# Performance work log

Hardware: AMD Instinct MI355X
Metric: run time of the kernel (lower is better)

Reference implementation:

```python
import jax, jax.numpy as jnp
import numpy as np

B, S, E, H, F = 8, 1024, 1024, 16, 4096
D = E // H  # head_dim = 64
EPS = 1e-5


def setup_inputs() -> dict:
    key = jax.random.key(0)
    ks = jax.random.split(key, 12)
    s = 0.02
    return {
        "x": jax.random.normal(ks[0], (B, S, E), dtype=jnp.float32),
        # per-head projections (shared across heads), torch stores [out,in]; we use [in,out]
        "Wq": jax.random.normal(ks[1], (D, D), dtype=jnp.float32) * s,
        "Wk": jax.random.normal(ks[2], (D, D), dtype=jnp.float32) * s,
        "Wv": jax.random.normal(ks[3], (D, D), dtype=jnp.float32) * s,
        "Wo": jax.random.normal(ks[4], (E, E), dtype=jnp.float32) * s,
        "bo": jnp.zeros((E,), dtype=jnp.float32),
        "W1": jax.random.normal(ks[5], (E, F), dtype=jnp.float32) * s,
        "b1": jnp.zeros((F,), dtype=jnp.float32),
        "W2": jax.random.normal(ks[6], (F, E), dtype=jnp.float32) * s,
        "b2": jnp.zeros((E,), dtype=jnp.float32),
        "g1": jnp.ones((E,), dtype=jnp.float32),
        "beta1": jnp.zeros((E,), dtype=jnp.float32),
        "g2": jnp.ones((E,), dtype=jnp.float32),
        "beta2": jnp.zeros((E,), dtype=jnp.float32),
    }


def _layer_norm(x, g, b):
    m = jnp.mean(x, axis=-1, keepdims=True)
    v = jnp.mean(jnp.square(x - m), axis=-1, keepdims=True)
    return (x - m) * jax.lax.rsqrt(v + EPS) * g + b


def reference(x, Wq, Wk, Wv, Wo, bo, W1, b1, W2, b2, g1, beta1, g2, beta2):
    b, s, e = x.shape
    # --- attention sublayer (pre-norm) ---
    nx = _layer_norm(x, g1, beta1)
    h = nx.reshape(b, s, H, D)              # [B,S,H,D]
    q = h @ Wq                               # per-head linear, weight shared over heads
    k = h @ Wk
    v = h @ Wv
    energy = jnp.einsum('bqhd,bkhd->bhqk', q, k)  # full [B,H,S,S] scores
    mask = jnp.tril(jnp.ones((s, s), dtype=bool))
    energy = jnp.where(mask, energy, -jnp.inf)
    att = jax.nn.softmax(energy / jnp.sqrt(jnp.float32(e)), axis=-1)  # NOTE: scale by sqrt(embed_dim)
    o = jnp.einsum('bhqk,bkhd->bqhd', att, v).reshape(b, s, e)
    x = x + (o @ Wo + bo)
    # --- MLP sublayer (pre-norm); dropout is identity in eval ---
    nx = _layer_norm(x, g2, beta2)
    x = x + (jax.nn.relu(nx @ W1 + b1) @ W2 + b2)
    return x
```

## Files before the change

kernel.cpp:

```cpp
#include <hip/hip_runtime.h>

typedef unsigned short u16;
typedef __attribute__((ext_vector_type(4))) float f4;
typedef __attribute__((ext_vector_type(8))) short s8v;
typedef __attribute__((ext_vector_type(4))) unsigned short u16x4;

#define DEVINL __device__ __forceinline__

DEVINL float b2f(u16 u) { union { unsigned i; float f; } x; x.i = ((unsigned)u) << 16; return x.f; }
DEVINL u16 f2b(float f) {
  union { float f; unsigned i; } x; x.f = f;
  unsigned r = 0x7FFFu + ((x.i >> 16) & 1u);
  return (u16)((x.i + r) >> 16);
}

#define GLD_LDS16(g, l)                                                        \
  __builtin_amdgcn_global_load_lds((__attribute__((address_space(1))) void*)(g), \
                                   (__attribute__((address_space(3))) void*)(l), 16, 0, 0)

__global__ __launch_bounds__(256) void k_transpose_all(
    const float* __restrict__ Wo, const float* __restrict__ W1,
    const float* __restrict__ W2, const float* __restrict__ Wq,
    const float* __restrict__ Wk, const float* __restrict__ Wv,
    u16* __restrict__ WoT, u16* __restrict__ W1T, u16* __restrict__ W2T,
    u16* __restrict__ WqT, u16* __restrict__ WkT, u16* __restrict__ WvT) {
  int id = blockIdx.x;
  const float* in;
  u16* out;
  int R, C, bx, by;
  if (id < 1024) {
    in = Wo; out = WoT; R = 1024; C = 1024; bx = id & 31; by = id >> 5;
  } else if (id < 5120) {
    int t = id - 1024;
    in = W1; out = W1T; R = 1024; C = 4096; bx = t & 127; by = t >> 7;
  } else if (id < 9216) {
    int t = id - 5120;
    in = W2; out = W2T; R = 4096; C = 1024; bx = t & 31; by = t >> 5;
  } else {
    int t = id - 9216;
    int z = t >> 2;
    in = z == 0 ? Wq : (z == 1 ? Wk : Wv);
    out = z == 0 ? WqT : (z == 1 ? WkT : WvT);
    R = 64; C = 64; bx = t & 1; by = (t >> 1) & 1;
  }
  __shared__ float tt[32][33];
  int tx = threadIdx.x & 31, ty = threadIdx.x >> 5;
  int c0 = bx * 32, r0 = by * 32;
#pragma unroll
  for (int i = 0; i < 32; i += 8)
    tt[ty + i][tx] = in[(long)(r0 + ty + i) * C + (c0 + tx)];
  __syncthreads();
#pragma unroll
  for (int i = 0; i < 32; i += 8)
    out[(long)(c0 + ty + i) * R + (r0 + tx)] = f2b(tt[tx][ty + i]);
}

__global__ __launch_bounds__(256) void k_vtrans(const u16* __restrict__ v, u16* __restrict__ vt) {
  __shared__ u16 t[64][72];
  int bh = blockIdx.x, b = bh >> 4, h = bh & 15;
  int s0 = blockIdx.y * 64;
  int tid = threadIdx.x;
#pragma unroll
  for (int p = 0; p < 2; ++p) {
    int idx = p * 256 + tid;
    int sl = idx >> 3, c8 = (idx & 7) * 8;
    *(s8v*)(&t[sl][c8]) = *(const s8v*)(v + (((long)(b * 1024 + s0 + sl) * 16 + h) * 64) + c8);
  }
  __syncthreads();
#pragma unroll
  for (int p = 0; p < 2; ++p) {
    int idx = p * 256 + tid;
    int d = idx >> 3, c8 = (idx & 7) * 8;
    s8v o;
#pragma unroll
    for (int e = 0; e < 8; ++e) o[e] = (short)t[c8 + e][d];
    *(s8v*)(vt + ((long)bh * 64 + d) * 1024 + s0 + c8) = o;
  }
}

__global__ __launch_bounds__(256) void k_layernorm(const float* __restrict__ x,
                                                   const float* __restrict__ g,
                                                   const float* __restrict__ be,
                                                   u16* __restrict__ out) {
  long row = blockIdx.x;
  int tid = threadIdx.x;
  f4 v = ((const f4*)(x + row * 1024))[tid];
  float s = v[0] + v[1] + v[2] + v[3];
  float s2 = v[0] * v[0] + v[1] * v[1] + v[2] * v[2] + v[3] * v[3];
#pragma unroll
  for (int off = 32; off > 0; off >>= 1) {
    s += __shfl_down(s, off, 64);
    s2 += __shfl_down(s2, off, 64);
  }
  __shared__ float red[8];
  int wv = tid >> 6, ln = tid & 63;
  if (ln == 0) { red[wv] = s; red[4 + wv] = s2; }
  __syncthreads();
  s = red[0] + red[1] + red[2] + red[3];
  s2 = red[4] + red[5] + red[6] + red[7];
  float mean = s * (1.0f / 1024.0f);
  float var = s2 * (1.0f / 1024.0f) - mean * mean;
  float rs = rsqrtf(var + 1e-5f);
  f4 gg = ((const f4*)g)[tid];
  f4 bb = ((const f4*)be)[tid];
  u16x4 o;
#pragma unroll
  for (int i = 0; i < 4; ++i) o[i] = f2b((v[i] - mean) * rs * gg[i] + bb[i]);
  ((u16x4*)(out + row * 1024))[tid] = o;
}

__global__ __launch_bounds__(256) void k_qkv(const u16* __restrict__ nx, const u16* __restrict__ WqT,
                                             const u16* __restrict__ WkT, const u16* __restrict__ WvT,
                                             u16* __restrict__ q, u16* __restrict__ k,
                                             u16* __restrict__ v) {
  int tid = threadIdx.x, lane = tid & 63, wave = tid >> 6;
  int quad = lane >> 4, l16 = lane & 15;
  long rbase = (long)blockIdx.x * 64 + wave * 16;
  s8v a0 = *(const s8v*)(nx + (rbase + l16) * 64 + quad * 8);
  s8v a1 = *(const s8v*)(nx + (rbase + l16) * 64 + 32 + quad * 8);
  const u16* Ws[3] = {WqT, WkT, WvT};
  u16* Os[3] = {q, k, v};
#pragma unroll
  for (int t = 0; t < 3; ++t) {
#pragma unroll
    for (int j = 0; j < 4; ++j) {
      s8v b0 = *(const s8v*)(Ws[t] + (j * 16 + l16) * 64 + quad * 8);
      s8v b1 = *(const s8v*)(Ws[t] + (j * 16 + l16) * 64 + 32 + quad * 8);
      f4 acc = {0.f, 0.f, 0.f, 0.f};
      acc = __builtin_amdgcn_mfma_f32_16x16x32_bf16(a0, b0, acc, 0, 0, 0);
      acc = __builtin_amdgcn_mfma_f32_16x16x32_bf16(a1, b1, acc, 0, 0, 0);
#pragma unroll
      for (int r = 0; r < 4; ++r)
        Os[t][(rbase + quad * 4 + r) * 64 + j * 16 + l16] = f2b(acc[r]);
    }
  }
}

__global__ __launch_bounds__(256) void k_attn_mfma(const u16* __restrict__ q,
                                                   const u16* __restrict__ kk,
                                                   const u16* __restrict__ vt,
                                                   u16* __restrict__ o) {
  constexpr int LDK = 72;
  __shared__ u16 Ks[64 * LDK];
  __shared__ u16 Vt[64 * LDK];
  __shared__ u16 Ps[4][16 * LDK];
  int tid = threadIdx.x, lane = tid & 63, wave = tid >> 6;
  int quad = lane >> 4, l16 = lane & 15;
  int b = blockIdx.x >> 4, h = blockIdx.x & 15;
  int qi = (int)gridDim.y - 1 - (int)blockIdx.y;
  int q0 = qi * 64 + wave * 16;

  const u16* qp = q + (((long)(b * 1024 + q0 + l16)) * 16 + h) * 64;
  s8v aq0 = *(const s8v*)(qp + quad * 8);
  s8v aq1 = *(const s8v*)(qp + 32 + quad * 8);

  f4 O[4];
  float m_[4], l_[4];
#pragma unroll
  for (int jd = 0; jd < 4; ++jd) O[jd] = f4{0.f, 0.f, 0.f, 0.f};
#pragma unroll
  for (int r = 0; r < 4; ++r) { m_[r] = -__builtin_inff(); l_[r] = 0.f; }

  for (int kt = 0; kt <= qi; ++kt) {
    __syncthreads();
#pragma unroll
    for (int p = 0; p < 2; ++p) {
      int idx = p * 256 + tid;
      int row = idx >> 3, c8 = (idx & 7) * 8;
      *(s8v*)(Ks + row * LDK + c8) =
          *(const s8v*)(kk + (((long)(b * 1024 + kt * 64 + row)) * 16 + h) * 64 + c8);
      *(s8v*)(Vt + row * LDK + c8) =
          *(const s8v*)(vt + ((long)blockIdx.x * 64 + row) * 1024 + kt * 64 + c8);
    }
    __syncthreads();

    f4 sf[4];
    __builtin_amdgcn_s_setprio(1);
#pragma unroll
    for (int jn = 0; jn < 4; ++jn) {
      s8v b0 = *(const s8v*)(Ks + (jn * 16 + l16) * LDK + quad * 8);
      s8v b1 = *(const s8v*)(Ks + (jn * 16 + l16) * LDK + 32 + quad * 8);
      f4 acc = f4{0.f, 0.f, 0.f, 0.f};
      acc = __builtin_amdgcn_mfma_f32_16x16x32_bf16(aq0, b0, acc, 0, 0, 0);
      acc = __builtin_amdgcn_mfma_f32_16x16x32_bf16(aq1, b1, acc, 0, 0, 0);
      sf[jn] = acc;
    }
    __builtin_amdgcn_s_setprio(0);
    bool diag = (kt == qi);
    float rm[4];
#pragma unroll
    for (int r = 0; r < 4; ++r) rm[r] = -__builtin_inff();
#pragma unroll
    for (int jn = 0; jn < 4; ++jn)
#pragma unroll
      for (int r = 0; r < 4; ++r) {
        float v = sf[jn][r] * 0.03125f;
        if (diag && (jn * 16 + l16 > wave * 16 + quad * 4 + r)) v = -__builtin_inff();
        sf[jn][r] = v;
        rm[r] = fmaxf(rm[r], v);
      }
#pragma unroll
    for (int off = 1; off < 16; off <<= 1)
#pragma unroll
      for (int r = 0; r < 4; ++r) rm[r] = fmaxf(rm[r], __shfl_xor(rm[r], off, 64));
    float alpha[4], rs[4];
#pragma unroll
    for (int r = 0; r < 4; ++r) {
      float mn = fmaxf(m_[r], rm[r]);
      alpha[r] = __expf(m_[r] - mn);
      m_[r] = mn;
      rs[r] = 0.f;
    }
#pragma unroll
    for (int jn = 0; jn < 4; ++jn)
#pragma unroll
      for (int r = 0; r < 4; ++r) {
        float p = __expf(sf[jn][r] - m_[r]);
        rs[r] += p;
        Ps[wave][(quad * 4 + r) * LDK + jn * 16 + l16] = f2b(p);
      }
#pragma unroll
    for (int off = 1; off < 16; off <<= 1)
#pragma unroll
      for (int r = 0; r < 4; ++r) rs[r] += __shfl_xor(rs[r], off, 64);
#pragma unroll
    for (int r = 0; r < 4; ++r) l_[r] = l_[r] * alpha[r] + rs[r];
#pragma unroll
    for (int jd = 0; jd < 4; ++jd)
#pragma unroll
      for (int r = 0; r < 4; ++r) O[jd][r] *= alpha[r];
    asm volatile("s_waitcnt lgkmcnt(0)" ::: "memory");
    s8v p0 = *(const s8v*)(&Ps[wave][l16 * LDK + quad * 8]);
    s8v p1 = *(const s8v*)(&Ps[wave][l16 * LDK + 32 + quad * 8]);
    __builtin_amdgcn_s_setprio(1);
#pragma unroll
    for (int jd = 0; jd < 4; ++jd) {
      s8v b0 = *(const s8v*)(Vt + (jd * 16 + l16) * LDK + quad * 8);
      s8v b1 = *(const s8v*)(Vt + (jd * 16 + l16) * LDK + 32 + quad * 8);
      O[jd] = __builtin_amdgcn_mfma_f32_16x16x32_bf16(p0, b0, O[jd], 0, 0, 0);
      O[jd] = __builtin_amdgcn_mfma_f32_16x16x32_bf16(p1, b1, O[jd], 0, 0, 0);
    }
    __builtin_amdgcn_s_setprio(0);
  }
#pragma unroll
  for (int r = 0; r < 4; ++r) {
    float inv = 1.0f / l_[r];
    u16* op = o + (((long)(b * 1024 + q0 + quad * 4 + r)) * 16 + h) * 64;
#pragma unroll
    for (int jd = 0; jd < 4; ++jd) op[jd * 16 + l16] = f2b(O[jd][r] * inv);
  }
}

template <int EPI>
__global__ __launch_bounds__(512) void k_gemm256(const u16* __restrict__ A,
                                                 const u16* __restrict__ BT,
                                                 const float* __restrict__ bias,
                                                 const float* __restrict__ resid,
                                                 void* __restrict__ outp, int M, int N, int K,
                                                 int lda) {
  __shared__ __align__(16) u16 S[65536];
  int tid = threadIdx.x, lane = tid & 63, wave = tid >> 6;
  int l16 = lane & 15, quad = lane >> 4;
  int wm = wave >> 2, wn = wave & 3;
  long bm = blockIdx.x, bn = blockIdx.y;
  int z = blockIdx.z;

  int rl = l16 & 7;
  int c0 = 8 * (quad ^ rl);
  int c1 = 8 * ((quad ^ 4) ^ rl);
  int rowA = (wm * 64 + l16) * 64;
  int rowB = (wn * 32 + l16) * 64;

  int Lb = tid * 16;
  int Ls = Lb ^ (((Lb >> 7) & 7) << 4);
  int r_ = Ls >> 7, kin = (Ls & 127) >> 1;
  const u16* pA = A + (bm * 256 + r_) * (long)lda + kin + (long)z * K;
  const u16* pB = BT + (bn * 256 + r_) * (long)lda + kin + (long)z * K;

  f4 acc[4][4][2];
#pragma unroll
  for (int q = 0; q < 4; ++q)
#pragma unroll
    for (int mi = 0; mi < 4; ++mi)
#pragma unroll
      for (int nj = 0; nj < 2; ++nj) acc[q][mi][nj] = f4{0.f, 0.f, 0.f, 0.f};
  s8v aF[4][2], bF[2][2][2];

#define BAR asm volatile("s_barrier" ::: "memory")
#define LGK0 asm volatile("s_waitcnt lgkmcnt(0)" ::: "memory")
#define WVM4 asm volatile("s_waitcnt vmcnt(4)" ::: "memory")
#define WVM0 asm volatile("s_waitcnt vmcnt(0)" ::: "memory")

#define STAGE(mat, half, t, buf)                                               \
  do {                                                                         \
    const u16* g_ = ((mat) ? pB : pA) + (long)(half) * 128 * lda + (t) * 64;   \
    char* l_ = ((char*)S) + ((buf) * 32768 + (mat) * 16384 + (half) * 8192) * 2 + wave * 1024; \
    GLD_LDS16(g_, l_);                                                         \
    GLD_LDS16(g_ + 64 * (long)lda, l_ + 8192);                                 \
  } while (0)

#define LDA(buf, mh)                                                           \
  do {                                                                         \
    const u16* p_ = S + (buf) * 32768 + (mh) * 8192 + rowA;                    \
    _Pragma("unroll") for (int mi = 0; mi < 4; ++mi) {                         \
      aF[mi][0] = *(const s8v*)(p_ + mi * 1024 + c0);                          \
      aF[mi][1] = *(const s8v*)(p_ + mi * 1024 + c1);                          \
    }                                                                          \
  } while (0)

#define LDB(buf, nh, set)                                                      \
  do {                                                                         \
    const u16* p_ = S + (buf) * 32768 + 16384 + (nh) * 8192 + rowB;            \
    _Pragma("unroll") for (int nj = 0; nj < 2; ++nj) {                         \
      bF[set][nj][0] = *(const s8v*)(p_ + nj * 1024 + c0);                     \
      bF[set][nj][1] = *(const s8v*)(p_ + nj * 1024 + c1);                     \
    }                                                                          \
  } while (0)

#define MM(q)                                                                  \
  do {                                                                         \
    _Pragma("unroll") for (int mi = 0; mi < 4; ++mi)                           \
        _Pragma("unroll") for (int nj = 0; nj < 2; ++nj) {                     \
      acc[q][mi][nj] = __builtin_amdgcn_mfma_f32_16x16x32_bf16(                \
          aF[mi][0], bF[(q) & 1][nj][0], acc[q][mi][nj], 0, 0, 0);             \
      acc[q][mi][nj] = __builtin_amdgcn_mfma_f32_16x16x32_bf16(                \
          aF[mi][1], bF[(q) & 1][nj][1], acc[q][mi][nj], 0, 0, 0);             \
    }                                                                          \
  } while (0)

#define PHASES(t, LAST)                                                        \
  LDA(0, 0); LDB(0, 0, 0); STAGE(0, 1, (t) + 1, 1);                            \
  BAR; LGK0; __builtin_amdgcn_s_setprio(1); MM(0); __builtin_amdgcn_s_setprio(0); BAR; \
  LDB(0, 1, 1); STAGE(1, 1, (t) + 1, 1);                                       \
  BAR; LGK0; __builtin_amdgcn_s_setprio(1); MM(1); __builtin_amdgcn_s_setprio(0); BAR; \
  LDA(0, 1); if (!(LAST)) STAGE(0, 0, (t) + 2, 0);                             \
  BAR; LGK0; __builtin_amdgcn_s_setprio(1); MM(2); __builtin_amdgcn_s_setprio(0); BAR; \
  if (!(LAST)) STAGE(1, 0, (t) + 2, 0);                                        \
  __builtin_amdgcn_s_setprio(1); MM(3); __builtin_amdgcn_s_setprio(0);         \
  if (LAST) { WVM0; } else { WVM4; }                                           \
  BAR;                                                                         \
  LDA(1, 0); LDB(1, 0, 0); if (!(LAST)) STAGE(0, 1, (t) + 2, 0);               \
  BAR; LGK0; __builtin_amdgcn_s_setprio(1); MM(0); __builtin_amdgcn_s_setprio(0); BAR; \
  LDB(1, 1, 1); if (!(LAST)) STAGE(1, 1, (t) + 2, 0);                          \
  BAR; LGK0; __builtin_amdgcn_s_setprio(1); MM(1); __builtin_amdgcn_s_setprio(0); BAR; \
  LDA(1, 1); if (!(LAST)) STAGE(0, 0, (t) + 3, 1);                             \
  BAR; LGK0; __builtin_amdgcn_s_setprio(1); MM(2); __builtin_amdgcn_s_setprio(0); BAR; \
  if (!(LAST)) STAGE(1, 0, (t) + 3, 1);                                        \
  __builtin_amdgcn_s_setprio(1); MM(3); __builtin_amdgcn_s_setprio(0);         \
  if (!(LAST)) { WVM4; BAR; }

  STAGE(0, 0, 0, 0);
  STAGE(1, 0, 0, 0);
  STAGE(0, 1, 0, 0);
  STAGE(1, 1, 0, 0);
  STAGE(0, 0, 1, 1);
  STAGE(1, 0, 1, 1);
  WVM4; BAR;

  int NI = K >> 7;
  for (int i = 0; i < NI - 1; ++i) {
    int t = 2 * i;
    PHASES(t, 0);
  }
  {
    int t = 2 * (NI - 1);
    PHASES(t, 1);
  }

#undef PHASES
#undef MM
#undef LDB
#undef LDA
#undef STAGE
#undef WVM0
#undef WVM4
#undef LGK0
#undef BAR

  float* P0 = (EPI == 0) ? ((float*)outp + (long)z * M * N) : nullptr;
#pragma unroll
  for (int q = 0; q < 4; ++q) {
    int mh = q >> 1, nh = q & 1;
#pragma unroll
    for (int mi = 0; mi < 4; ++mi) {
#pragma unroll
      for (int nj = 0; nj < 2; ++nj) {
        long row = bm * 256 + mh * 128 + wm * 64 + mi * 16 + quad * 4;
        int col = (int)bn * 256 + nh * 128 + wn * 32 + nj * 16 + l16;
        float bcol = 0.f;
        if (EPI != 0) bcol = bias[col];
#pragma unroll
        for (int rr = 0; rr < 4; ++rr) {
          float val = acc[q][mi][nj][rr] + bcol;
          if (EPI == 0) {
            P0[(row + rr) * (long)N + col] = val;
          } else if (EPI == 1) {
            ((u16*)outp)[(row + rr) * (long)N + col] = f2b(val > 0.f ? val : 0.f);
          } else {
            ((float*)outp)[(row + rr) * (long)N + col] =
                resid[(row + rr) * (long)N + col] + val;
          }
        }
      }
    }
  }
}

__global__ __launch_bounds__(512) void k_gemm256n128(const u16* __restrict__ A,
                                                     const u16* __restrict__ BT,
                                                     const float* __restrict__ bias,
                                                     const float* __restrict__ resid,
                                                     float* __restrict__ outp,
                                                     int M, int N, int K, int lda) {
  __shared__ __align__(16) u16 S[49152];
  int tid = threadIdx.x, lane = tid & 63, wave = tid >> 6;
  int l16 = lane & 15, quad = lane >> 4;
  int wm = wave >> 1, wn = wave & 1;
  long bm = blockIdx.x, bn = blockIdx.y;

  int rl = l16 & 7;
  int c0 = 8 * (quad ^ rl);
  int c1 = 8 * ((quad ^ 4) ^ rl);
  int rowA = (wm >> 1) * 8192 + ((wm & 1) * 64 + l16) * 64;
  int rowB = 16384 + (wn * 64 + l16) * 64;

  int Lb = tid * 16;
  int Ls = Lb ^ (((Lb >> 7) & 7) << 4);
  int r_ = Ls >> 7, kin = (Ls & 127) >> 1;
  const u16* pA = A + (bm * 256 + r_) * (long)lda + kin;
  const u16* pB = BT + (bn * 128 + r_) * (long)lda + kin;

  f4 acc[4][4];
#pragma unroll
  for (int mi = 0; mi < 4; ++mi)
#pragma unroll
    for (int nj = 0; nj < 4; ++nj) acc[mi][nj] = f4{0.f, 0.f, 0.f, 0.f};
  s8v aF[4][2], bF[2][2];

#define BAR asm volatile("s_barrier" ::: "memory")
#define LGK0 asm volatile("s_waitcnt lgkmcnt(0)" ::: "memory")
#define WVM4 asm volatile("s_waitcnt vmcnt(4)" ::: "memory")
#define WVM0 asm volatile("s_waitcnt vmcnt(0)" ::: "memory")

#define STAGEA(t, buf)                                                         \
  do {                                                                         \
    const u16* g_ = pA + (t) * 64;                                             \
    char* l_ = ((char*)S) + (buf) * 49152 + wave * 1024;                       \
    GLD_LDS16(g_, l_);                                                         \
    GLD_LDS16(g_ + 64 * (long)lda, l_ + 8192);                                 \
    GLD_LDS16(g_ + 128 * (long)lda, l_ + 16384);                               \
    GLD_LDS16(g_ + 192 * (long)lda, l_ + 24576);                               \
  } while (0)

#define STAGEB(t, buf)                                                         \
  do {                                                                         \
    const u16* g_ = pB + (t) * 64;                                             \
    char* l_ = ((char*)S) + (buf) * 49152 + 32768 + wave * 1024;               \
    GLD_LDS16(g_, l_);                                                         \
    GLD_LDS16(g_ + 64 * (long)lda, l_ + 8192);                                 \
  } while (0)

#define LDAn(buf)                                                              \
  do {                                                                         \
    const u16* p_ = S + (buf) * 24576 + rowA;                                  \
    _Pragma("unroll") for (int mi = 0; mi < 4; ++mi) {                         \
      aF[mi][0] = *(const s8v*)(p_ + mi * 1024 + c0);                          \
      aF[mi][1] = *(const s8v*)(p_ + mi * 1024 + c1);                          \
    }                                                                          \
  } while (0)

#define LDBn(buf, nh)                                                          \
  do {                                                                         \
    const u16* p_ = S + (buf) * 24576 + rowB + (nh) * 2048;                    \
    _Pragma("unroll") for (int nj2 = 0; nj2 < 2; ++nj2) {                      \
      bF[nj2][0] = *(const s8v*)(p_ + nj2 * 1024 + c0);                        \
      bF[nj2][1] = *(const s8v*)(p_ + nj2 * 1024 + c1);                        \
    }                                                                          \
  } while (0)

#define MMn(nh)                                                                \
  do {                                                                         \
    _Pragma("unroll") for (int mi = 0; mi < 4; ++mi)                           \
        _Pragma("unroll") for (int nj2 = 0; nj2 < 2; ++nj2) {                  \
      acc[mi][(nh) * 2 + nj2] = __builtin_amdgcn_mfma_f32_16x16x32_bf16(       \
          aF[mi][0], bF[nj2][0], acc[mi][(nh) * 2 + nj2], 0, 0, 0);            \
      acc[mi][(nh) * 2 + nj2] = __builtin_amdgcn_mfma_f32_16x16x32_bf16(       \
          aF[mi][1], bF[nj2][1], acc[mi][(nh) * 2 + nj2], 0, 0, 0);            \
    }                                                                          \
  } while (0)

#define PHASES(t, LAST)                                                        \
  LDAn(0); LDBn(0, 0); STAGEB((t) + 1, 1);                                     \
  BAR; LGK0; __builtin_amdgcn_s_setprio(1); MMn(0); __builtin_amdgcn_s_setprio(0); BAR; \
  LDBn(0, 1); if (!(LAST)) STAGEA((t) + 2, 0);                                 \
  BAR; LGK0; __builtin_amdgcn_s_setprio(1); MMn(1); __builtin_amdgcn_s_setprio(0); \
  if (LAST) { WVM0; } else { WVM4; }                                           \
  BAR;                                                                         \
  LDAn(1); LDBn(1, 0); if (!(LAST)) STAGEB((t) + 2, 0);                        \
  BAR; LGK0; __builtin_amdgcn_s_setprio(1); MMn(0); __builtin_amdgcn_s_setprio(0); BAR; \
  LDBn(1, 1); if (!(LAST)) STAGEA((t) + 3, 1);                                 \
  BAR; LGK0; __builtin_amdgcn_s_setprio(1); MMn(1); __builtin_amdgcn_s_setprio(0); \
  if (!(LAST)) { WVM4; }                                                       \
  BAR;

  STAGEA(0, 0);
  STAGEB(0, 0);
  STAGEA(1, 1);
  WVM4; BAR;

  int NI = K >> 7;
  for (int i = 0; i < NI - 1; ++i) {
    int t = 2 * i;
    PHASES(t, 0);
  }
  {
    int t = 2 * (NI - 1);
    PHASES(t, 1);
  }

#undef PHASES
#undef MMn
#undef LDBn
#undef LDAn
#undef STAGEB
#undef STAGEA
#undef WVM0
#undef WVM4
#undef LGK0
#undef BAR

#pragma unroll
  for (int mi = 0; mi < 4; ++mi) {
#pragma unroll
    for (int nj = 0; nj < 4; ++nj) {
      long row = bm * 256 + wm * 64 + mi * 16 + quad * 4;
      int col = (int)bn * 128 + wn * 64 + nj * 16 + l16;
      float bcol = bias[col];
#pragma unroll
      for (int rr = 0; rr < 4; ++rr) {
        outp[(row + rr) * (long)N + col] =
            resid[(row + rr) * (long)N + col] + acc[mi][nj][rr] + bcol;
      }
    }
  }
}

extern "C" void kernel_launch(void* const* d_in, const int* in_sizes, int n_in, void* d_out,
                              int out_size, void* d_ws, size_t ws_size, hipStream_t stream) {
  const float* x = (const float*)d_in[0];
  const float* Wq = (const float*)d_in[1];
  const float* Wk = (const float*)d_in[2];
  const float* Wv = (const float*)d_in[3];
  const float* Wo = (const float*)d_in[4];
  const float* bo = (const float*)d_in[5];
  const float* W1 = (const float*)d_in[6];
  const float* b1 = (const float*)d_in[7];
  const float* W2 = (const float*)d_in[8];
  const float* b2 = (const float*)d_in[9];
  const float* g1 = (const float*)d_in[10];
  const float* be1 = (const float*)d_in[11];
  const float* g2 = (const float*)d_in[12];
  const float* be2 = (const float*)d_in[13];

  char* ws = (char*)d_ws;
  const size_t MB = 1ull << 20;
  u16* nx = (u16*)(ws + 0);
  u16* qb = (u16*)(ws + 16 * MB);
  u16* kb = (u16*)(ws + 32 * MB);
  u16* vb = (u16*)(ws + 48 * MB);
  float* x1 = (float*)(ws + 64 * MB);
  u16* h1 = (u16*)(ws + 96 * MB);
  u16* vtr = (u16*)(ws + 96 * MB);
  u16* WoT = (u16*)(ws + 160 * MB);
  u16* W1T = (u16*)(ws + 162 * MB);
  u16* W2T = (u16*)(ws + 170 * MB);
  u16* WqT = (u16*)(ws + 178 * MB);
  u16* WkT = WqT + 64 * 64;
  u16* WvT = WkT + 64 * 64;
  u16* ob = nx;
  u16* nx2 = qb;

  k_transpose_all<<<9228, 256, 0, stream>>>(Wo, W1, W2, Wq, Wk, Wv, WoT, W1T, W2T, WqT, WkT, WvT);

  k_layernorm<<<8192, 256, 0, stream>>>(x, g1, be1, nx);
  k_qkv<<<2048, 256, 0, stream>>>(nx, WqT, WkT, WvT, qb, kb, vb);
  k_vtrans<<<dim3(128, 16), 256, 0, stream>>>(vb, vtr);
  k_attn_mfma<<<dim3(128, 16), 256, 0, stream>>>(qb, kb, vtr, ob);
  k_gemm256n128<<<dim3(32, 8), 512, 0, stream>>>(ob, WoT, bo, x, x1, 8192, 1024, 1024, 1024);

  k_layernorm<<<8192, 256, 0, stream>>>(x1, g2, be2, nx2);
  k_gemm256<1><<<dim3(32, 16, 1), 512, 0, stream>>>(nx2, W1T, b1, nullptr, h1, 8192, 4096, 1024, 1024);
  k_gemm256n128<<<dim3(32, 8), 512, 0, stream>>>(h1, W2T, b2, x1, (float*)d_out, 8192, 1024, 4096, 4096);
}
```

Baseline: 393.0 us.

## Fuse first layernorm into QKV projection and double-buffer K/V tiles in attention

The first layernorm is folded into the QKV kernel. Each wave normalizes one full 1024-wide row and writes bf16 to shared memory as the 64-wide head slices, so the intermediate normalized tensor never makes a round trip through global memory. The attention kernel now uses double-buffered K/V shared tiles: the next tile is prefetched into registers before the compute and stored to the alternate buffer afterward, leaving one barrier per iteration. This aims to hide global load latency behind the MFMA work, at the cost of double the LDS, which may reduce occupancy.

```diff
diff --git a/kernel.cpp b/kernel.cpp
--- a/kernel.cpp
+++ b/kernel.cpp
@@ -109,15 +109,47 @@
   ((u16x4*)(out + row * 1024))[tid] = o;
 }
 
-__global__ __launch_bounds__(256) void k_qkv(const u16* __restrict__ nx, const u16* __restrict__ WqT,
-                                             const u16* __restrict__ WkT, const u16* __restrict__ WvT,
-                                             u16* __restrict__ q, u16* __restrict__ k,
-                                             u16* __restrict__ v) {
+__global__ __launch_bounds__(256) void k_ln_qkv(
+    const float* __restrict__ x, const float* __restrict__ g, const float* __restrict__ be,
+    const u16* __restrict__ WqT, const u16* __restrict__ WkT, const u16* __restrict__ WvT,
+    u16* __restrict__ q, u16* __restrict__ k, u16* __restrict__ v) {
+  constexpr int LDP = 72;
+  __shared__ u16 A[64 * LDP];
   int tid = threadIdx.x, lane = tid & 63, wave = tid >> 6;
   int quad = lane >> 4, l16 = lane & 15;
+  long xrow = (long)blockIdx.x * 4 + wave;
+  const f4* xp = (const f4*)(x + xrow * 1024);
+  const f4* gp = (const f4*)g;
+  const f4* bp = (const f4*)be;
+  f4 vv[4];
+  float s = 0.f, s2 = 0.f;
+#pragma unroll
+  for (int j = 0; j < 4; ++j) {
+    vv[j] = xp[lane * 4 + j];
+#pragma unroll
+    for (int e = 0; e < 4; ++e) { s += vv[j][e]; s2 += vv[j][e] * vv[j][e]; }
+  }
+#pragma unroll
+  for (int off = 1; off < 64; off <<= 1) {
+    s += __shfl_xor(s, off, 64);
+    s2 += __shfl_xor(s2, off, 64);
+  }
+  float mean = s * (1.0f / 1024.0f);
+  float var = s2 * (1.0f / 1024.0f) - mean * mean;
+  float rs = rsqrtf(var + 1e-5f);
+  u16* ap = &A[(wave * 16 + (lane >> 2)) * LDP + (lane & 3) * 16];
+#pragma unroll
+  for (int j = 0; j < 4; ++j) {
+    f4 gg = gp[lane * 4 + j], bb = bp[lane * 4 + j];
+    u16x4 o;
+#pragma unroll
+    for (int e = 0; e < 4; ++e) o[e] = f2b((vv[j][e] - mean) * rs * gg[e] + bb[e]);
+    *(u16x4*)(ap + j * 4) = o;
+  }
+  __syncthreads();
+  s8v a0 = *(const s8v*)(&A[(wave * 16 + l16) * LDP + quad * 8]);
+  s8v a1 = *(const s8v*)(&A[(wave * 16 + l16) * LDP + 32 + quad * 8]);
   long rbase = (long)blockIdx.x * 64 + wave * 16;
-  s8v a0 = *(const s8v*)(nx + (rbase + l16) * 64 + quad * 8);
-  s8v a1 = *(const s8v*)(nx + (rbase + l16) * 64 + 32 + quad * 8);
   const u16* Ws[3] = {WqT, WkT, WvT};
   u16* Os[3] = {q, k, v};
 #pragma unroll
@@ -141,8 +173,8 @@
                                                    const u16* __restrict__ vt,
                                                    u16* __restrict__ o) {
   constexpr int LDK = 72;
-  __shared__ u16 Ks[64 * LDK];
-  __shared__ u16 Vt[64 * LDK];
+  __shared__ u16 Ks[2][64 * LDK];
+  __shared__ u16 Vt[2][64 * LDK];
   __shared__ u16 Ps[4][16 * LDK];
   int tid = threadIdx.x, lane = tid & 63, wave = tid >> 6;
   int quad = lane >> 4, l16 = lane & 15;
@@ -154,6 +186,11 @@
   s8v aq0 = *(const s8v*)(qp + quad * 8);
   s8v aq1 = *(const s8v*)(qp + 32 + quad * 8);
 
+  int srow0 = tid >> 3, sc8 = (tid & 7) * 8;
+  int srow1 = srow0 + 32;
+  const u16* kb_ = kk + (long)b * 1048576 + h * 64;
+  const u16* vb_ = vt + (long)blockIdx.x * 65536;
+
   f4 O[4];
   float m_[4], l_[4];
 #pragma unroll
@@ -161,25 +198,34 @@
 #pragma unroll
   for (int r = 0; r < 4; ++r) { m_[r] = -__builtin_inff(); l_[r] = 0.f; }
 
+  s8v rk0 = *(const s8v*)(kb_ + (long)srow0 * 1024 + sc8);
+  s8v rk1 = *(const s8v*)(kb_ + (long)srow1 * 1024 + sc8);
+  s8v rv0 = *(const s8v*)(vb_ + (long)srow0 * 1024 + sc8);
+  s8v rv1 = *(const s8v*)(vb_ + (long)srow1 * 1024 + sc8);
+  *(s8v*)(&Ks[0][srow0 * LDK + sc8]) = rk0;
+  *(s8v*)(&Ks[0][srow1 * LDK + sc8]) = rk1;
+  *(s8v*)(&Vt[0][srow0 * LDK + sc8]) = rv0;
+  *(s8v*)(&Vt[0][srow1 * LDK + sc8]) = rv1;
+
   for (int kt = 0; kt <= qi; ++kt) {
+    int cur = kt & 1;
+    if (kt < qi) {
+      long ko = (long)(kt + 1) * 64;
+      rk0 = *(const s8v*)(kb_ + (ko + srow0) * 1024 + sc8);
+      rk1 = *(const s8v*)(kb_ + (ko + srow1) * 1024 + sc8);
+      rv0 = *(const s8v*)(vb_ + (long)srow0 * 1024 + (kt + 1) * 64 + sc8);
+      rv1 = *(const s8v*)(vb_ + (long)srow1 * 1024 + (kt + 1) * 64 + sc8);
+    }
     __syncthreads();
-#pragma unroll
-    for (int p = 0; p < 2; ++p) {
-      int idx = p * 256 + tid;
-      int row = idx >> 3, c8 = (idx & 7) * 8;
-      *(s8v*)(Ks + row * LDK + c8) =
-          *(const s8v*)(kk + (((long)(b * 1024 + kt * 64 + row)) * 16 + h) * 64 + c8);
-      *(s8v*)(Vt + row * LDK + c8) =
-          *(const s8v*)(vt + ((long)blockIdx.x * 64 + row) * 1024 + kt * 64 + c8);
-    }
-    __syncthreads();
-
+
+    const u16* Kc = Ks[cur];
+    const u16* Vc = Vt[cur];
     f4 sf[4];
     __builtin_amdgcn_s_setprio(1);
 #pragma unroll
     for (int jn = 0; jn < 4; ++jn) {
-      s8v b0 = *(const s8v*)(Ks + (jn * 16 + l16) * LDK + quad * 8);
-      s8v b1 = *(const s8v*)(Ks + (jn * 16 + l16) * LDK + 32 + quad * 8);
+      s8v b0 = *(const s8v*)(Kc + (jn * 16 + l16) * LDK + quad * 8);
+      s8v b1 = *(const s8v*)(Kc + (jn * 16 + l16) * LDK + 32 + quad * 8);
       f4 acc = f4{0.f, 0.f, 0.f, 0.f};
       acc = __builtin_amdgcn_mfma_f32_16x16x32_bf16(aq0, b0, acc, 0, 0, 0);
       acc = __builtin_amdgcn_mfma_f32_16x16x32_bf16(aq1, b1, acc, 0, 0, 0);
@@ -235,12 +281,20 @@
     __builtin_amdgcn_s_setprio(1);
 #pragma unroll
     for (int jd = 0; jd < 4; ++jd) {
-      s8v b0 = *(const s8v*)(Vt + (jd * 16 + l16) * LDK + quad * 8);
-      s8v b1 = *(const s8v*)(Vt + (jd * 16 + l16) * LDK + 32 + quad * 8);
+      s8v b0 = *(const s8v*)(Vc + (jd * 16 + l16) * LDK + quad * 8);
+      s8v b1 = *(const s8v*)(Vc + (jd * 16 + l16) * LDK + 32 + quad * 8);
       O[jd] = __builtin_amdgcn_mfma_f32_16x16x32_bf16(p0, b0, O[jd], 0, 0, 0);
       O[jd] = __builtin_amdgcn_mfma_f32_16x16x32_bf16(p1, b1, O[jd], 0, 0, 0);
     }
     __builtin_amdgcn_s_setprio(0);
+
+    if (kt < qi) {
+      int nb = cur ^ 1;
+      *(s8v*)(&Ks[nb][srow0 * LDK + sc8]) = rk0;
+      *(s8v*)(&Ks[nb][srow1 * LDK + sc8]) = rk1;
+      *(s8v*)(&Vt[nb][srow0 * LDK + sc8]) = rv0;
+      *(s8v*)(&Vt[nb][srow1 * LDK + sc8]) = rv1;
+    }
   }
 #pragma unroll
   for (int r = 0; r < 4; ++r) {
@@ -582,8 +636,7 @@
 
   k_transpose_all<<<9228, 256, 0, stream>>>(Wo, W1, W2, Wq, Wk, Wv, WoT, W1T, W2T, WqT, WkT, WvT);
 
-  k_layernorm<<<8192, 256, 0, stream>>>(x, g1, be1, nx);
-  k_qkv<<<2048, 256, 0, stream>>>(nx, WqT, WkT, WvT, qb, kb, vb);
+  k_ln_qkv<<<2048, 256, 0, stream>>>(x, g1, be1, WqT, WkT, WvT, qb, kb, vb);
   k_vtrans<<<dim3(128, 16), 256, 0, stream>>>(vb, vtr);
   k_attn_mfma<<<dim3(128, 16), 256, 0, stream>>>(qb, kb, vtr, ob);
   k_gemm256n128<<<dim3(32, 8), 512, 0, stream>>>(ob, WoT, bo, x, x1, 8192, 1024, 1024, 1024);
```

Result: no change. 386.5 us (-1.7%).
